# Kernel optimization log

Measured on AMD Instinct MI355X. Metric: run time of the kernel, lower is better.

Reference implementation:

```python
import jax, jax.numpy as jnp
import numpy as np

AR_COEF = 0.01
TAR_COEF = 0.01
LN_EPS = 1e-5


def setup_inputs() -> dict:
    key = jax.random.key(0)
    ks = jax.random.split(key, 8)
    B, T, D, E, H, A = 32, 512, 256, 1024, 1024, 64
    def rn(k, shape, fan_in):
        return jax.random.normal(k, shape, jnp.float32) * (1.0 / np.sqrt(fan_in))
    return {
        "obs": jax.random.normal(ks[0], (B, T, D), jnp.float32),
        "hxs": jnp.zeros((B, H), jnp.float32),
        "cxs": jnp.zeros((B, H), jnp.float32),
        "W1": rn(ks[1], (E, D), D), "b1": jnp.zeros((E,), jnp.float32),
        "W2": rn(ks[2], (E, E), E), "b2": jnp.zeros((E,), jnp.float32),
        "W_ih": rn(ks[3], (4 * H, E), E),
        "W_hh": rn(ks[4], (4 * H, H), H),
        "b_ih": jnp.zeros((4 * H,), jnp.float32),
        "b_hh": jnp.zeros((4 * H,), jnp.float32),
        "ln_g": jnp.ones((H,), jnp.float32), "ln_b": jnp.zeros((H,), jnp.float32),
        "Wa": rn(ks[5], (A, H), H), "ba": jnp.zeros((A,), jnp.float32),
        "Wc": rn(ks[6], (1, H), H), "bc": jnp.zeros((1,), jnp.float32),
    }


def reference(obs, hxs, cxs, W1, b1, W2, b2, W_ih, W_hh, b_ih, b_hh,
              ln_g, ln_b, Wa, ba, Wc, bc):
    # obs encoder (identity) + 2-layer SiLU MLP encoder
    enc = jax.nn.silu(obs @ W1.T + b1)        # (B,T,E)
    enc = jax.nn.silu(enc @ W2.T + b2)        # (B,T,E)

    # precompute input-to-gate contributions; gates in PyTorch order i,f,g,o
    x_gates = enc @ W_ih.T + (b_ih + b_hh)    # (B,T,4H)
    xg = jnp.transpose(x_gates, (1, 0, 2))    # (T,B,4H)

    def step(carry, xt):
        h, c = carry
        g = xt + h @ W_hh.T                   # (B,4H)
        i, f, gg, o = jnp.split(g, 4, axis=-1)
        c = jax.nn.sigmoid(f) * c + jax.nn.sigmoid(i) * jnp.tanh(gg)
        h = jax.nn.sigmoid(o) * jnp.tanh(c)
        return (h, c), h

    (h_n, c_n), outs = jax.lax.scan(step, (hxs, cxs), xg)
    out = jnp.transpose(outs, (1, 0, 2))      # (B,T,H)

    # LayerNorm
    mu = out.mean(-1, keepdims=True)
    var = ((out - mu) ** 2).mean(-1, keepdims=True)
    out_ln = (out - mu) * jax.lax.rsqrt(var + LN_EPS) * ln_g + ln_b

    ar_loss = (out_ln ** 2).mean() * AR_COEF
    tar_loss = ((out_ln[:, 1:, :] - out_ln[:, :-1, :]) ** 2).mean() * TAR_COEF

    logits = out_ln @ Wa.T + ba               # (B,T,A)
    values = (out_ln @ Wc.T + bc)[..., 0]     # (B,T)
    return logits, values, h_n, c_n, ar_loss, tar_loss
```

## Files before the change

kernel.cpp:

```cpp
#include <hip/hip_runtime.h>

typedef __attribute__((ext_vector_type(8))) short bf16x8;
typedef __attribute__((ext_vector_type(8))) unsigned short u16x8;
typedef __attribute__((ext_vector_type(4))) unsigned short u16x4;
typedef __attribute__((ext_vector_type(4))) float f32x4;

#define NB 32
#define NT 512
#define ND 256
#define NE 1024
#define NH 1024
#define LSTM_SMEM (131072 + 16640)

__device__ __forceinline__ float bf2f(unsigned short u){
  union { unsigned int i; float f; } w; w.i = ((unsigned int)u) << 16; return w.f;
}
__device__ __forceinline__ unsigned short f2bf(float f){
  union { float f; unsigned int i; } w; w.f = f;
  unsigned int r = (w.i >> 16) & 1u;
  return (unsigned short)((w.i + 0x7fffu + r) >> 16);
}

__device__ __forceinline__ f32x4 bypass_load_f32x4(const float* p){
  f32x4 r;
  asm volatile("global_load_dwordx4 %0, %1, off sc0 sc1" : "=v"(r) : "v"(p) : "memory");
  return r;
}
__device__ __forceinline__ int bypass_load_i32(const int* p){
  int r;
  asm volatile("global_load_dword %0, %1, off sc0 sc1\n\ts_waitcnt vmcnt(0)"
               : "=v"(r) : "v"(p) : "memory");
  return r;
}
__device__ __forceinline__ void bypass_store_f32x4(float* p, f32x4 v){
  asm volatile("global_store_dwordx4 %0, %1, off sc0 sc1" :: "v"(p), "v"(v) : "memory");
}

__device__ __forceinline__ void gload_lds16(const void* g, void* l){
  __builtin_amdgcn_global_load_lds(
      (const __attribute__((address_space(1))) void*)g,
      (__attribute__((address_space(3))) void*)l, 16, 0, 0);
}

__device__ __forceinline__ unsigned pkbf(float a, float b){
  unsigned r; asm("v_cvt_pk_bf16_f32 %0, %1, %2" : "=v"(r) : "v"(a), "v"(b)); return r;
}
__device__ __forceinline__ void make_frags(f32x4 x0, f32x4 x1, bf16x8& hi, bf16x8& lo){
  union Uv { unsigned u[4]; bf16x8 v; } H, L;
#pragma unroll
  for (int w=0; w<4; w++){
    float a = (w<2) ? x0[w*2]   : x1[(w-2)*2];
    float b = (w<2) ? x0[w*2+1] : x1[(w-2)*2+1];
    unsigned hw = pkbf(a, b);
    H.u[w] = hw;
    union { unsigned u; float f; } e0, e1;
    e0.u = hw << 16; e1.u = hw & 0xffff0000u;
    L.u[w] = pkbf(a - e0.f, b - e1.f);
  }
  hi = H.v; lo = L.v;
}

__global__ void mega_prep(const float* __restrict__ W1, const float* __restrict__ W2,
                          const float* __restrict__ Wih,
                          const float* __restrict__ Wa, const float* __restrict__ Wc,
                          const float* __restrict__ ba, const float* __restrict__ bc,
                          const float* __restrict__ b_ih, const float* __restrict__ b_hh,
                          const float* __restrict__ hxs, const float* __restrict__ cxs,
                          unsigned short* __restrict__ W1_b, unsigned short* __restrict__ W2_b,
                          unsigned short* __restrict__ Wih_b, unsigned short* __restrict__ Whead_b,
                          float* __restrict__ bias_heads, float* __restrict__ bias_xg,
                          float* __restrict__ h_bufs, float* __restrict__ c_buf,
                          int* __restrict__ cnt)
{
  long i0 = (long)blockIdx.x*256 + threadIdx.x;
  long stride = (long)gridDim.x*256;
  for (long i=i0; i<(long)NE*ND;   i+=stride) W1_b[i]  = f2bf(W1[i]);
  for (long i=i0; i<(long)NE*NE;   i+=stride) W2_b[i]  = f2bf(W2[i]);
  for (long i=i0; i<(long)4*NH*NE; i+=stride) Wih_b[i] = f2bf(Wih[i]);
  for (long i=i0; i<128*1024; i+=stride){
    int n = (int)(i>>10), k = (int)(i&1023);
    Whead_b[i] = f2bf(n<64 ? Wa[i] : (n==64 ? Wc[k] : 0.f));
  }
  for (long i=i0; i<4096; i+=stride) bias_xg[i] = b_ih[i] + b_hh[i];
  for (long i=i0; i<65;   i+=stride) bias_heads[i] = (i<64) ? ba[i] : bc[0];
  for (long i=i0; i<NB*NH; i+=stride){ h_bufs[i] = hxs[i]; c_buf[i] = cxs[i]; }
  for (long i=i0; i<1024; i+=stride) cnt[i] = 0;
}

__global__ void f2b_obs_chunk(const float* __restrict__ obs, unsigned short* __restrict__ dst,
                              int lgTc, int t0){
  const int Tc = 1 << lgTc;
  const long n = (long)NB * Tc * ND;
  long i = (long)blockIdx.x*blockDim.x + threadIdx.x;
  long stride = (long)gridDim.x*blockDim.x;
  for (; i < n; i += stride){
    long lr = i >> 8;
    int col = (int)(i & 255);
    long gr = (lr >> lgTc)*NT + t0 + (lr & (Tc-1));
    dst[i] = f2bf(obs[gr*ND + col]);
  }
}

__global__ void sentinel_kernel(float* __restrict__ out){ out[0] = 1.0e6f; }

#define GEMM_COMPUTE(P) { \
  bf16x8 af[4], bfr[4]; \
  _Pragma("unroll") for (int f=0; f<4; f++){ \
    af[f]  = *(const bf16x8*)&As[P][(wm*64 + f*16 + fr)*32 + kf]; \
    bfr[f] = *(const bf16x8*)&Bs[P][(wn*64 + f*16 + fr)*32 + kf]; } \
  _Pragma("unroll") for (int i=0;i<4;i++) \
    _Pragma("unroll") for (int j=0;j<4;j++) \
      acc[i][j] = __builtin_amdgcn_mfma_f32_16x16x32_bf16(af[i], bfr[j], acc[i][j], 0, 0, 0); }

template<int SILU, int HEADS>
__global__ __launch_bounds__(256)
void gemm_bt(const unsigned short* __restrict__ A, const unsigned short* __restrict__ Bw,
             const float* __restrict__ bias, unsigned short* __restrict__ C,
             float* __restrict__ oLogits, float* __restrict__ oValues,
             int K, int N, int Nreal)
{
  __shared__ __align__(16) unsigned short As[2][128*32];
  __shared__ __align__(16) unsigned short Bs[2][128*32];
  const int tid = threadIdx.x;
  const int lane = tid & 63;
  const int w = tid >> 6;
  const int wm = w >> 1, wn = w & 1;
  const int m0 = blockIdx.x * 128, n0 = blockIdx.y * 128;
  f32x4 acc[4][4];
#pragma unroll
  for (int i=0;i<4;i++)
#pragma unroll
    for (int j=0;j<4;j++){ f32x4 z = {0.f,0.f,0.f,0.f}; acc[i][j] = z; }
  const int fr = lane & 15;
  const int kf = (lane >> 4) * 8;
  const int r0 = tid >> 2, s0 = tid & 3;
  const unsigned short* gA0 = A  + (size_t)(m0+r0)*K    + s0*8;
  const unsigned short* gA1 = A  + (size_t)(m0+r0+64)*K + s0*8;
  const unsigned short* gB0 = Bw + (size_t)(n0+r0)*K    + s0*8;
  const unsigned short* gB1 = Bw + (size_t)(n0+r0+64)*K + s0*8;

  auto stage = [&](int p, int k0){
    char* a = (char*)&As[p][0] + w*1024;
    char* b = (char*)&Bs[p][0] + w*1024;
    gload_lds16(gA0 + k0, a);
    gload_lds16(gA1 + k0, a + 4096);
    gload_lds16(gB0 + k0, b);
    gload_lds16(gB1 + k0, b + 4096);
  };

  stage(0, 0);
  asm volatile("s_waitcnt vmcnt(0)" ::: "memory");
  __syncthreads();
  int cur = 0;
  for (int k0 = 32; k0 < K; k0 += 32){
    stage(cur ^ 1, k0);
    GEMM_COMPUTE(cur);
    asm volatile("s_waitcnt vmcnt(0)" ::: "memory");
    __syncthreads();
    cur ^= 1;
  }
  GEMM_COMPUTE(cur);

  const int mb = (lane >> 4) * 4;
  const int nb = lane & 15;
#pragma unroll
  for (int i=0;i<4;i++)
#pragma unroll
    for (int j=0;j<4;j++)
#pragma unroll
      for (int r=0;r<4;r++){
        int m = m0 + wm*64 + i*16 + mb + r;
        int n = n0 + wn*64 + j*16 + nb;
        if (HEADS && n >= Nreal) continue;
        float v = acc[i][j][r] + bias[n];
        if (SILU) v = v / (1.f + expf(-v));
        if (!HEADS) {
          C[(size_t)m*N + n] = f2bf(v);
        } else {
          if (n < 64) oLogits[(size_t)m*64 + n] = v;
          else if (n == 64) oValues[m] = v;
        }
      }
}

__global__ __launch_bounds__(512)
void lstm_mfma(const unsigned short* __restrict__ xg, const float* __restrict__ Whh,
               float* __restrict__ h_bufs, float* __restrict__ c_buf,
               unsigned short* __restrict__ hist, float* __restrict__ dh, float* __restrict__ dc,
               int* __restrict__ cnt, int t0, int t1, int Tc)
{
  extern __shared__ char smem[];
  unsigned short* Wf = (unsigned short*)smem;
  float* red = (float*)(smem + 131072);
  const int wg = blockIdx.x;
  const int bh = wg & 1, ug = wg >> 1;
  const int b0 = bh*16, n0w = ug*8;
  const int tid = threadIdx.x;
  const int lane = tid & 63;
  const int wv = tid >> 6;
  const int fr = lane & 15;
  const int q8 = (lane >> 4) * 8;

  for (int s = tid; s < 8192; s += 512){
    int term = s >> 12, kt = (s >> 7) & 31, nt = (s >> 6) & 1, l = s & 63;
    int r = nt*16 + (l & 15);
    int g = r >> 3, uu2 = r & 7;
    const float* src = Whh + (size_t)(g*NH + n0w + uu2)*NH + kt*32 + (l>>4)*8;
    u16x8 o;
#pragma unroll
    for (int j=0;j<8;j++){
      float wv_ = src[j];
      unsigned short hi = f2bf(wv_);
      o[j] = (term==0) ? hi : f2bf(wv_ - bf2f(hi));
    }
    *(u16x8*)&Wf[(size_t)s*8] = o;
  }

  const int bl = tid >> 3;
  const int uu = tid & 7;
  float c_reg = 0.f, h_keep = 0.f;
  if (tid < 128) c_reg = c_buf[(b0 + bl)*NH + n0w + uu];
  __syncthreads();

  for (int t = t0; t < t1; t++){
    const float* hb = h_bufs + (size_t)(t & 1)*(NB*NH);
    float* hb_next  = h_bufs + (size_t)((t+1)&1)*(NB*NH);
    const int tl = t - t0;

    float xgv[4] = {0.f,0.f,0.f,0.f};
    if (tid < 128){
      size_t xbase = ((size_t)(b0+bl)*Tc + tl)*4096 + n0w + uu;
#pragma unroll
      for (int g=0; g<4; g++) xgv[g] = bf2f(xg[xbase + g*1024]);
    }

    if (wv == 0){
      const int target = 256*t;
      while (true){
        int v = 0;
        if (lane < 16) v = bypass_load_i32(&cnt[lane*64]);
        v += __shfl_xor(v,1); v += __shfl_xor(v,2); v += __shfl_xor(v,4);
        v += __shfl_xor(v,8); v += __shfl_xor(v,16); v += __shfl_xor(v,32);
        if (v >= target) break;
        __builtin_amdgcn_s_sleep(1);
      }
    }
    __syncthreads();

    f32x4 hv[8];
#pragma unroll
    for (int ks=0; ks<4; ks++){
      const float* p = hb + (size_t)(b0 + fr)*NH + (wv*4 + ks)*32 + q8;
      hv[ks*2]   = bypass_load_f32x4(p);
      hv[ks*2+1] = bypass_load_f32x4(p + 4);
    }
    asm volatile("s_waitcnt vmcnt(0)" ::: "memory");
    __builtin_amdgcn_sched_barrier(0);

    bf16x8 ahi[4], alo[4];
#pragma unroll
    for (int ks=0; ks<4; ks++) make_frags(hv[2*ks], hv[2*ks+1], ahi[ks], alo[ks]);

    f32x4 acc[2];
    { f32x4 z = {0.f,0.f,0.f,0.f}; acc[0] = z; acc[1] = z; }
#pragma unroll
    for (int ks=0; ks<4; ks++){
      int kt = wv*4 + ks;
#pragma unroll
      for (int nt=0; nt<2; nt++){
        bf16x8 bhi = *(const bf16x8*)&Wf[kt*1024 + nt*512 + lane*8];
        bf16x8 blo = *(const bf16x8*)&Wf[32768 + kt*1024 + nt*512 + lane*8];
        acc[nt] = __builtin_amdgcn_mfma_f32_16x16x32_bf16(ahi[ks], bhi, acc[nt], 0,0,0);
        acc[nt] = __builtin_amdgcn_mfma_f32_16x16x32_bf16(ahi[ks], blo, acc[nt], 0,0,0);
        acc[nt] = __builtin_amdgcn_mfma_f32_16x16x32_bf16(alo[ks], bhi, acc[nt], 0,0,0);
      }
    }

#pragma unroll
    for (int nt=0; nt<2; nt++)
#pragma unroll
      for (int r4=0; r4<4; r4++)
        red[((lane>>4)*4 + r4)*260 + (nt*16 + fr)*8 + wv] = acc[nt][r4];
    __syncthreads();

    if (tid < 128){
      float gate[4];
#pragma unroll
      for (int g=0; g<4; g++){
        int base = bl*260 + (g*8 + uu)*8;
        f32x4 s0 = *(const f32x4*)&red[base];
        f32x4 s1 = *(const f32x4*)&red[base+4];
        gate[g] = ((s0[0]+s0[1])+(s0[2]+s0[3])) + ((s1[0]+s1[1])+(s1[2]+s1[3])) + xgv[g];
      }
      float iv = 1.f/(1.f+expf(-gate[0]));
      float fv = 1.f/(1.f+expf(-gate[1]));
      float gv = tanhf(gate[2]);
      float ov = 1.f/(1.f+expf(-gate[3]));
      float c_new = fv*c_reg + iv*gv;
      float h_new = ov*tanhf(c_new);
      c_reg = c_new; h_keep = h_new;
      float h0 = __shfl(h_new, (lane & 60) + 0);
      float h1 = __shfl(h_new, (lane & 60) + 1);
      float h2 = __shfl(h_new, (lane & 60) + 2);
      float h3 = __shfl(h_new, (lane & 60) + 3);
      if ((uu & 3) == 0){
        f32x4 hvv = { h0, h1, h2, h3 };
        bypass_store_f32x4(hb_next + (size_t)(b0+bl)*NH + n0w + uu, hvv);
        u16x4 hp; hp[0]=f2bf(h0); hp[1]=f2bf(h1); hp[2]=f2bf(h2); hp[3]=f2bf(h3);
        *(u16x4*)&hist[((size_t)(b0+bl)*Tc + tl)*NH + n0w + uu] = hp;
      }
    }
    __syncthreads();
    if (tid == 0) atomicAdd(&cnt[(wg & 15)*64], 1);
  }
  if (tid < 128){
    c_buf[(b0+bl)*NH + n0w + uu] = c_reg;
    if (t1 == NT){ dh[(b0+bl)*NH + n0w + uu] = h_keep; dc[(b0+bl)*NH + n0w + uu] = c_reg; }
  }
}

#define SEL4(A0,A1,A2,A3) ((kc&2)?((kc&1)?(A3):(A2)):((kc&1)?(A1):(A0)))

__global__ __launch_bounds__(512)
void lstm_valu(const unsigned short* __restrict__ xg, const float* __restrict__ Whh,
               float* __restrict__ h_bufs, float* __restrict__ c_buf,
               unsigned short* __restrict__ hist, float* __restrict__ dh, float* __restrict__ dc,
               int* __restrict__ cnt, int t0, int t1, int Tc)
{
  __shared__ __align__(16) float Wl[16*1024];
  const int wg = blockIdx.x;
  const int n0w = wg * 4;
  const int tid = threadIdx.x;
  const int lane = tid & 63;
  const int wv = tid >> 6;
  const int kc = lane & 15;
  const int b = wv*4 + (lane >> 4);

  for (int i = tid*4; i < 16*1024; i += 2048){
    int r = i >> 10, k = i & 1023;
    int grow = (r>>2)*NH + n0w + (r&3);
    *(f32x4*)&Wl[i] = *(const f32x4*)&Whh[(size_t)grow*NH + k];
  }
  float c_reg = 0.f, h_keep = 0.f;
  if (kc < 4) c_reg = c_buf[b*NH + n0w + kc];
  __syncthreads();

  for (int t = t0; t < t1; t++){
    const float* hb = h_bufs + (size_t)(t&1)*(NB*NH);
    float* hb_next  = h_bufs + (size_t)((t+1)&1)*(NB*NH);
    const int tl = t - t0;
    float xgi=0.f, xgf=0.f, xgg=0.f, xgo=0.f;
    if (kc < 4){
      size_t xbase = ((size_t)b*Tc + tl)*4096 + n0w + kc;
      xgi = bf2f(xg[xbase]);
      xgf = bf2f(xg[xbase + 1024]);
      xgg = bf2f(xg[xbase + 2048]);
      xgo = bf2f(xg[xbase + 3072]);
    }
    if (wv == 0){
      const int target = 256*t;
      while (true){
        int v = 0;
        if (lane < 16) v = bypass_load_i32(&cnt[lane*64]);
        v += __shfl_xor(v,1); v += __shfl_xor(v,2); v += __shfl_xor(v,4);
        v += __shfl_xor(v,8); v += __shfl_xor(v,16); v += __shfl_xor(v,32);
        if (v >= target) break;
        __builtin_amdgcn_s_sleep(1);
      }
    }
    __syncthreads();

    f32x4 hq[16];
    const float* hrow = hb + (size_t)b*NH + kc*4;
#pragma unroll
    for (int kk=0; kk<16; kk++) hq[kk] = bypass_load_f32x4(hrow + kk*64);

    float acc[16];
#pragma unroll
    for (int r=0;r<16;r++) acc[r] = 0.f;
#pragma unroll
    for (int g=0; g<4; g++){
      if (g==0){ asm volatile("s_waitcnt vmcnt(12)" ::: "memory"); }
      else if (g==1){ asm volatile("s_waitcnt vmcnt(8)" ::: "memory"); }
      else if (g==2){ asm volatile("s_waitcnt vmcnt(4)" ::: "memory"); }
      else { asm volatile("s_waitcnt vmcnt(0)" ::: "memory"); }
      __builtin_amdgcn_sched_barrier(0);
#pragma unroll
      for (int kq=0; kq<4; kq++){
        const int kk = g*4 + kq;
#pragma unroll
        for (int r=0;r<16;r++){
          f32x4 wq = *(const f32x4*)&Wl[r*1024 + kk*64 + kc*4];
          acc[r] = fmaf(wq[0],hq[kk][0], fmaf(wq[1],hq[kk][1],
                   fmaf(wq[2],hq[kk][2], fmaf(wq[3],hq[kk][3], acc[r]))));
        }
      }
    }
#pragma unroll
    for (int r=0;r<16;r++){
      float v = acc[r];
      v += __shfl_xor(v, 1);
      v += __shfl_xor(v, 2);
      v += __shfl_xor(v, 4);
      v += __shfl_xor(v, 8);
      acc[r] = v;
    }
    float gi = SEL4(acc[0], acc[1], acc[2], acc[3])   + xgi;
    float gf = SEL4(acc[4], acc[5], acc[6], acc[7])   + xgf;
    float gg = SEL4(acc[8], acc[9], acc[10], acc[11]) + xgg;
    float go = SEL4(acc[12],acc[13],acc[14],acc[15])  + xgo;
    float iv = 1.f/(1.f+expf(-gi));
    float fv = 1.f/(1.f+expf(-gf));
    float gv = tanhf(gg);
    float ov = 1.f/(1.f+expf(-go));
    float c_new = fv*c_reg + iv*gv;
    float h_new = ov*tanhf(c_new);
    if (kc < 4){ c_reg = c_new; h_keep = h_new; }
    const int base = lane & 48;
    float h0 = __shfl(h_new, base + 0);
    float h1 = __shfl(h_new, base + 1);
    float h2 = __shfl(h_new, base + 2);
    float h3 = __shfl(h_new, base + 3);
    if (kc == 0){
      f32x4 hvv = { h0, h1, h2, h3 };
      bypass_store_f32x4(hb_next + (size_t)b*NH + n0w, hvv);
      u16x4 hp;
      hp[0] = f2bf(h0); hp[1] = f2bf(h1); hp[2] = f2bf(h2); hp[3] = f2bf(h3);
      *(u16x4*)&hist[((size_t)b*Tc + tl)*NH + n0w] = hp;
    }
    asm volatile("s_waitcnt vmcnt(0)" ::: "memory");
    __syncthreads();
    if (tid == 0) atomicAdd(&cnt[(wg & 15) * 64], 1);
  }
  if (kc < 4){
    c_buf[b*NH + n0w + kc] = c_reg;
    if (t1 == NT){ dh[b*NH + n0w + kc] = h_keep; dc[b*NH + n0w + kc] = c_reg; }
  }
}

__global__ __launch_bounds__(256)
void ln_chunk(const unsigned short* __restrict__ X, const float* __restrict__ gam, const float* __restrict__ bet,
              unsigned short* __restrict__ Y, int lgTc, int t0)
{
  const int row = blockIdx.x;
  const int Tc = 1 << lgTc;
  const int bl = row >> lgTc, tl = row & (Tc-1);
  const long grow = (long)bl*NT + t0 + tl;
  const int tid = threadIdx.x;
  u16x4 xv = *(const u16x4*)&X[(size_t)row*NH + tid*4];
  float v0 = bf2f(xv[0]), v1 = bf2f(xv[1]), v2 = bf2f(xv[2]), v3 = bf2f(xv[3]);
  float s = v0+v1+v2+v3;
  s += __shfl_xor(s,1); s += __shfl_xor(s,2); s += __shfl_xor(s,4);
  s += __shfl_xor(s,8); s += __shfl_xor(s,16); s += __shfl_xor(s,32);
  __shared__ float red[8];
  if ((tid & 63) == 0) red[tid >> 6] = s;
  __syncthreads();
  float mean = (red[0]+red[1]+red[2]+red[3]) * (1.0f/NH);
  float d0 = v0-mean, d1 = v1-mean, d2 = v2-mean, d3 = v3-mean;
  float q = d0*d0 + d1*d1 + d2*d2 + d3*d3;
  q += __shfl_xor(q,1); q += __shfl_xor(q,2); q += __shfl_xor(q,4);
  q += __shfl_xor(q,8); q += __shfl_xor(q,16); q += __shfl_xor(q,32);
  if ((tid & 63) == 0) red[4 + (tid >> 6)] = q;
  __syncthreads();
  float var = (red[4]+red[5]+red[6]+red[7]) * (1.0f/NH);
  float rs = 1.f / sqrtf(var + 1e-5f);
  f32x4 gm = *(const f32x4*)&gam[tid*4];
  f32x4 bt = *(const f32x4*)&bet[tid*4];
  u16x4 ov;
  ov[0] = f2bf(d0*rs*gm[0] + bt[0]);
  ov[1] = f2bf(d1*rs*gm[1] + bt[1]);
  ov[2] = f2bf(d2*rs*gm[2] + bt[2]);
  ov[3] = f2bf(d3*rs*gm[3] + bt[3]);
  *(u16x4*)&Y[(size_t)grow*NH + tid*4] = ov;
}

__global__ __launch_bounds__(256)
void loss_partial(const unsigned short* __restrict__ Yu, float* __restrict__ partials)
{
  float ar = 0.f, tar = 0.f;
  long stride = (long)gridDim.x*256;
  for (long vv = (long)blockIdx.x*256 + threadIdx.x; vv < 2097152; vv += stride){
    long i = vv*8;
    int t = (int)((i >> 10) & 511);
    u16x8 y = *(const u16x8*)&Yu[i];
    float x[8];
#pragma unroll
    for (int q=0;q<8;q++){ x[q] = bf2f(y[q]); ar += x[q]*x[q]; }
    if (t > 0){
      u16x8 yp = *(const u16x8*)&Yu[i - 1024];
#pragma unroll
      for (int q=0;q<8;q++){ float d = x[q] - bf2f(yp[q]); tar += d*d; }
    }
  }
  ar += __shfl_xor(ar,1); ar += __shfl_xor(ar,2); ar += __shfl_xor(ar,4);
  ar += __shfl_xor(ar,8); ar += __shfl_xor(ar,16); ar += __shfl_xor(ar,32);
  tar += __shfl_xor(tar,1); tar += __shfl_xor(tar,2); tar += __shfl_xor(tar,4);
  tar += __shfl_xor(tar,8); tar += __shfl_xor(tar,16); tar += __shfl_xor(tar,32);
  __shared__ float red[16];
  int w = threadIdx.x >> 6;
  if ((threadIdx.x & 63) == 0){ red[w] = ar; red[8+w] = tar; }
  __syncthreads();
  if (threadIdx.x == 0){
    partials[blockIdx.x*2]   = red[0]+red[1]+red[2]+red[3];
    partials[blockIdx.x*2+1] = red[8]+red[9]+red[10]+red[11];
  }
}

__global__ __launch_bounds__(256)
void loss_final(const float* __restrict__ partials, float* __restrict__ oAr, float* __restrict__ oTar){
  double sa = 0.0, st = 0.0;
  for (int i = threadIdx.x; i < 1024; i += 256){ sa += (double)partials[2*i]; st += (double)partials[2*i+1]; }
  for (int m=1;m<64;m<<=1){ sa += __shfl_xor(sa, m); st += __shfl_xor(st, m); }
  __shared__ double rd[8];
  int w = threadIdx.x >> 6;
  if ((threadIdx.x & 63) == 0){ rd[w] = sa; rd[4+w] = st; }
  __syncthreads();
  if (threadIdx.x == 0){
    double a  = rd[0]+rd[1]+rd[2]+rd[3];
    double tt = rd[4]+rd[5]+rd[6]+rd[7];
    oAr[0]  = (float)(a  / 16777216.0 * 0.01);
    oTar[0] = (float)(tt / 16744448.0 * 0.01);
  }
}

extern "C" void kernel_launch(void* const* d_in, const int* in_sizes, int n_in,
                              void* d_out, int out_size, void* d_ws, size_t ws_size,
                              hipStream_t stream)
{
  const float* obs  = (const float*)d_in[0];
  const float* hxs  = (const float*)d_in[1];
  const float* cxs  = (const float*)d_in[2];
  const float* W1   = (const float*)d_in[3];
  const float* b1   = (const float*)d_in[4];
  const float* W2   = (const float*)d_in[5];
  const float* b2   = (const float*)d_in[6];
  const float* W_ih = (const float*)d_in[7];
  const float* W_hh = (const float*)d_in[8];
  const float* b_ih = (const float*)d_in[9];
  const float* b_hh = (const float*)d_in[10];
  const float* ln_g = (const float*)d_in[11];
  const float* ln_b = (const float*)d_in[12];
  const float* Wa   = (const float*)d_in[13];
  const float* ba   = (const float*)d_in[14];
  const float* Wc   = (const float*)d_in[15];
  const float* bc   = (const float*)d_in[16];

  char* ws = (char*)d_ws;
  size_t off = 0;
  auto alloc = [&](size_t bytes)->char*{
    char* p = ws + off;
    off = (off + bytes + 255) & ~(size_t)255;
    return p;
  };
  unsigned short* W1_b    = (unsigned short*)alloc((size_t)NE*ND*2);
  unsigned short* W2_b    = (unsigned short*)alloc((size_t)NE*NE*2);
  unsigned short* Wih_b   = (unsigned short*)alloc((size_t)4*NH*NE*2);
  unsigned short* Whead_b = (unsigned short*)alloc((size_t)128*NH*2);
  float* bias_heads       = (float*)alloc(65*4);
  float* bias_xg          = (float*)alloc(4096*4);
  unsigned short* outln_b = (unsigned short*)alloc((size_t)NB*NT*NH*2);
  float* h_bufs           = (float*)alloc((size_t)2*NB*NH*4);
  float* c_buf            = (float*)alloc((size_t)NB*NH*4);
  int*   cnt              = (int*)alloc(1024*4);
  float* partials         = (float*)alloc((size_t)1024*2*4);
  const size_t fixedEnd = off;

  int lg = -1;
  for (int L = 9; L >= 4; --L){
    size_t Mc = (size_t)NB << L;
    size_t per = Mc*ND*2 + 2*(Mc*NE*2) + Mc*4096*2 + Mc*NH*2 + 6*256;
    if (fixedEnd + per <= ws_size){ lg = L; break; }
  }
  if (lg < 0){ sentinel_kernel<<<1,1,0,stream>>>((float*)d_out); return; }
  const int Tc = 1 << lg;
  const int Mc = NB << lg;
  const int nChunks = NT >> lg;

  unsigned short* obs_c  = (unsigned short*)alloc((size_t)Mc*ND*2);
  unsigned short* enc1_c = (unsigned short*)alloc((size_t)Mc*NE*2);
  unsigned short* enc2_c = (unsigned short*)alloc((size_t)Mc*NE*2);
  unsigned short* xg_c   = (unsigned short*)alloc((size_t)Mc*4096*2);
  unsigned short* hist_c = (unsigned short*)alloc((size_t)Mc*NH*2);

  float* o = (float*)d_out;
  float* oLogits = o;
  float* oValues = o + (size_t)NB*NT*64;
  float* oH  = oValues + NB*NT;
  float* oC  = oH + NB*NH;
  float* oAr = oC + NB*NH;
  float* oTar= oAr + 1;

  mega_prep<<<2048,256,0,stream>>>(W1, W2, W_ih, Wa, Wc, ba, bc, b_ih, b_hh, hxs, cxs,
                                   W1_b, W2_b, Wih_b, Whead_b, bias_heads, bias_xg,
                                   h_bufs, c_buf, cnt);

  for (int c = 0; c < nChunks; ++c){
    int t0 = c << lg, t1 = t0 + Tc;
    f2b_obs_chunk<<<512,256,0,stream>>>(obs, obs_c, lg, t0);
    gemm_bt<1,0><<<dim3(Mc/128,8) ,256,0,stream>>>(obs_c,  W1_b,  b1,      enc1_c, nullptr, nullptr, ND, NE, NE);
    gemm_bt<1,0><<<dim3(Mc/128,8) ,256,0,stream>>>(enc1_c, W2_b,  b2,      enc2_c, nullptr, nullptr, NE, NE, NE);
    gemm_bt<0,0><<<dim3(Mc/128,32),256,0,stream>>>(enc2_c, Wih_b, bias_xg, xg_c,   nullptr, nullptr, NE, 4096, 4096);

    (void)hipGetLastError();
    lstm_mfma<<<256,512,LSTM_SMEM,stream>>>(xg_c, W_hh, h_bufs, c_buf, hist_c, oH, oC, cnt, t0, t1, Tc);
    if (hipGetLastError() != hipSuccess)
      lstm_valu<<<256,512,0,stream>>>(xg_c, W_hh, h_bufs, c_buf, hist_c, oH, oC, cnt, t0, t1, Tc);

    ln_chunk<<<Mc,256,0,stream>>>(hist_c, ln_g, ln_b, outln_b, lg, t0);
  }

  gemm_bt<0,1><<<dim3(128,1),256,0,stream>>>(outln_b, Whead_b, bias_heads, nullptr, oLogits, oValues, NH, 128, 65);
  loss_partial<<<1024,256,0,stream>>>(outln_b, partials);
  loss_final<<<1,256,0,stream>>>(partials, oAr, oTar);
}
```

Before: 2.617 ms.

## Replace global atomic counter barrier with per-block step flags and per-wave waits

The LSTM recurrence's inter-block barrier changes from atomic counters summed by one wave to per-workgroup flag words that store the completed step. Each wave polls only the 16 producer blocks whose h slices it reads, which drops a __syncthreads and the global all-to-all dependency. Gate work is spread across waves (16 lanes per wave) with a padded reduction buffer to reduce LDS bank conflicts. LayerNorm is rewritten to one row per wave with wider vector loads. The partial-dependency flags raise the risk of subtle memory-ordering bugs.

New measurement: 2.567 ms. About the same (-1.9%).

```diff
diff --git a/kernel.cpp b/kernel.cpp
--- a/kernel.cpp
+++ b/kernel.cpp
@@ -10,7 +10,7 @@
 #define ND 256
 #define NE 1024
 #define NH 1024
-#define LSTM_SMEM (131072 + 16640)
+#define LSTM_SMEM (131072 + 18432)
 
 __device__ __forceinline__ float bf2f(unsigned short u){
   union { unsigned int i; float f; } w; w.i = ((unsigned int)u) << 16; return w.f;
@@ -34,6 +34,9 @@
 }
 __device__ __forceinline__ void bypass_store_f32x4(float* p, f32x4 v){
   asm volatile("global_store_dwordx4 %0, %1, off sc0 sc1" :: "v"(p), "v"(v) : "memory");
+}
+__device__ __forceinline__ void bypass_store_i32(int* p, int v){
+  asm volatile("global_store_dword %0, %1, off sc0 sc1" :: "v"(p), "v"(v) : "memory");
 }
 
 __device__ __forceinline__ void gload_lds16(const void* g, void* l){
@@ -70,7 +73,7 @@
                           unsigned short* __restrict__ Wih_b, unsigned short* __restrict__ Whead_b,
                           float* __restrict__ bias_heads, float* __restrict__ bias_xg,
                           float* __restrict__ h_bufs, float* __restrict__ c_buf,
-                          int* __restrict__ cnt)
+                          int* __restrict__ flags)
 {
   long i0 = (long)blockIdx.x*256 + threadIdx.x;
   long stride = (long)gridDim.x*256;
@@ -84,7 +87,7 @@
   for (long i=i0; i<4096; i+=stride) bias_xg[i] = b_ih[i] + b_hh[i];
   for (long i=i0; i<65;   i+=stride) bias_heads[i] = (i<64) ? ba[i] : bc[0];
   for (long i=i0; i<NB*NH; i+=stride){ h_bufs[i] = hxs[i]; c_buf[i] = cxs[i]; }
-  for (long i=i0; i<1024; i+=stride) cnt[i] = 0;
+  for (long i=i0; i<8192; i+=stride) flags[i] = 0;
 }
 
 __global__ void f2b_obs_chunk(const float* __restrict__ obs, unsigned short* __restrict__ dst,
@@ -187,7 +190,7 @@
 void lstm_mfma(const unsigned short* __restrict__ xg, const float* __restrict__ Whh,
                float* __restrict__ h_bufs, float* __restrict__ c_buf,
                unsigned short* __restrict__ hist, float* __restrict__ dh, float* __restrict__ dc,
-               int* __restrict__ cnt, int t0, int t1, int Tc)
+               int* __restrict__ flags, int t0, int t1, int Tc)
 {
   extern __shared__ char smem[];
   unsigned short* Wf = (unsigned short*)smem;
@@ -216,10 +219,10 @@
     *(u16x8*)&Wf[(size_t)s*8] = o;
   }
 
-  const int bl = tid >> 3;
-  const int uu = tid & 7;
+  const int bl = wv*2 + (lane >> 3);
+  const int uu = lane & 7;
   float c_reg = 0.f, h_keep = 0.f;
-  if (tid < 128) c_reg = c_buf[(b0 + bl)*NH + n0w + uu];
+  if (lane < 16) c_reg = c_buf[(b0 + bl)*NH + n0w + uu];
   __syncthreads();
 
   for (int t = t0; t < t1; t++){
@@ -228,24 +231,24 @@
     const int tl = t - t0;
 
     float xgv[4] = {0.f,0.f,0.f,0.f};
-    if (tid < 128){
+    if (lane < 16){
       size_t xbase = ((size_t)(b0+bl)*Tc + tl)*4096 + n0w + uu;
 #pragma unroll
       for (int g=0; g<4; g++) xgv[g] = bf2f(xg[xbase + g*1024]);
     }
 
-    if (wv == 0){
-      const int target = 256*t;
+    {
+      const int pw = ((wv*16 + fr)*2 + bh) * 32;
       while (true){
-        int v = 0;
-        if (lane < 16) v = bypass_load_i32(&cnt[lane*64]);
-        v += __shfl_xor(v,1); v += __shfl_xor(v,2); v += __shfl_xor(v,4);
-        v += __shfl_xor(v,8); v += __shfl_xor(v,16); v += __shfl_xor(v,32);
-        if (v >= target) break;
+        int v = bypass_load_i32(&flags[pw]);
+        v = min(v, __shfl_xor(v, 1));
+        v = min(v, __shfl_xor(v, 2));
+        v = min(v, __shfl_xor(v, 4));
+        v = min(v, __shfl_xor(v, 8));
+        if (v >= t) break;
         __builtin_amdgcn_s_sleep(1);
       }
     }
-    __syncthreads();
 
     f32x4 hv[8];
 #pragma unroll
@@ -279,18 +282,21 @@
 #pragma unroll
     for (int nt=0; nt<2; nt++)
 #pragma unroll
-      for (int r4=0; r4<4; r4++)
-        red[((lane>>4)*4 + r4)*260 + (nt*16 + fr)*8 + wv] = acc[nt][r4];
+      for (int r4=0; r4<4; r4++){
+        int batch = (lane>>4)*4 + r4;
+        red[batch*288 + (nt*16 + fr)*9 + wv] = acc[nt][r4];
+      }
     __syncthreads();
 
-    if (tid < 128){
+    if (lane < 16){
       float gate[4];
 #pragma unroll
       for (int g=0; g<4; g++){
-        int base = bl*260 + (g*8 + uu)*8;
-        f32x4 s0 = *(const f32x4*)&red[base];
-        f32x4 s1 = *(const f32x4*)&red[base+4];
-        gate[g] = ((s0[0]+s0[1])+(s0[2]+s0[3])) + ((s1[0]+s1[1])+(s1[2]+s1[3])) + xgv[g];
+        const float* rp = &red[bl*288 + (g*8 + uu)*9];
+        float s = 0.f;
+#pragma unroll
+        for (int w8=0; w8<8; w8++) s += rp[w8];
+        gate[g] = s + xgv[g];
       }
       float iv = 1.f/(1.f+expf(-gate[0]));
       float fv = 1.f/(1.f+expf(-gate[1]));
@@ -299,11 +305,11 @@
       float c_new = fv*c_reg + iv*gv;
       float h_new = ov*tanhf(c_new);
       c_reg = c_new; h_keep = h_new;
-      float h0 = __shfl(h_new, (lane & 60) + 0);
-      float h1 = __shfl(h_new, (lane & 60) + 1);
-      float h2 = __shfl(h_new, (lane & 60) + 2);
-      float h3 = __shfl(h_new, (lane & 60) + 3);
-      if ((uu & 3) == 0){
+      float h0 = __shfl(h_new, (lane & ~3) + 0);
+      float h1 = __shfl(h_new, (lane & ~3) + 1);
+      float h2 = __shfl(h_new, (lane & ~3) + 2);
+      float h3 = __shfl(h_new, (lane & ~3) + 3);
+      if ((lane & 3) == 0){
         f32x4 hvv = { h0, h1, h2, h3 };
         bypass_store_f32x4(hb_next + (size_t)(b0+bl)*NH + n0w + uu, hvv);
         u16x4 hp; hp[0]=f2bf(h0); hp[1]=f2bf(h1); hp[2]=f2bf(h2); hp[3]=f2bf(h3);
@@ -311,9 +317,9 @@
       }
     }
     __syncthreads();
-    if (tid == 0) atomicAdd(&cnt[(wg & 15)*64], 1);
-  }
-  if (tid < 128){
+    if (tid == 0) bypass_store_i32(&flags[wg*32], t+1);
+  }
+  if (lane < 16){
     c_buf[(b0+bl)*NH + n0w + uu] = c_reg;
     if (t1 == NT){ dh[(b0+bl)*NH + n0w + uu] = h_keep; dc[(b0+bl)*NH + n0w + uu] = c_reg; }
   }
@@ -442,36 +448,46 @@
 void ln_chunk(const unsigned short* __restrict__ X, const float* __restrict__ gam, const float* __restrict__ bet,
               unsigned short* __restrict__ Y, int lgTc, int t0)
 {
-  const int row = blockIdx.x;
   const int Tc = 1 << lgTc;
+  const int row = blockIdx.x*4 + (threadIdx.x >> 6);
+  const int lane = threadIdx.x & 63;
   const int bl = row >> lgTc, tl = row & (Tc-1);
   const long grow = (long)bl*NT + t0 + tl;
-  const int tid = threadIdx.x;
-  u16x4 xv = *(const u16x4*)&X[(size_t)row*NH + tid*4];
-  float v0 = bf2f(xv[0]), v1 = bf2f(xv[1]), v2 = bf2f(xv[2]), v3 = bf2f(xv[3]);
-  float s = v0+v1+v2+v3;
+  u16x8 a0 = *(const u16x8*)&X[(size_t)row*NH + lane*16];
+  u16x8 a1 = *(const u16x8*)&X[(size_t)row*NH + lane*16 + 8];
+  float x[16];
+  float s = 0.f;
+#pragma unroll
+  for (int j=0;j<8;j++){ x[j] = bf2f(a0[j]); x[8+j] = bf2f(a1[j]); }
+#pragma unroll
+  for (int j=0;j<16;j++) s += x[j];
   s += __shfl_xor(s,1); s += __shfl_xor(s,2); s += __shfl_xor(s,4);
   s += __shfl_xor(s,8); s += __shfl_xor(s,16); s += __shfl_xor(s,32);
-  __shared__ float red[8];
-  if ((tid & 63) == 0) red[tid >> 6] = s;
-  __syncthreads();
-  float mean = (red[0]+red[1]+red[2]+red[3]) * (1.0f/NH);
-  float d0 = v0-mean, d1 = v1-mean, d2 = v2-mean, d3 = v3-mean;
-  float q = d0*d0 + d1*d1 + d2*d2 + d3*d3;
+  const float mean = s * (1.0f/NH);
+  float q = 0.f;
+#pragma unroll
+  for (int j=0;j<16;j++){ float d = x[j]-mean; q += d*d; }
   q += __shfl_xor(q,1); q += __shfl_xor(q,2); q += __shfl_xor(q,4);
   q += __shfl_xor(q,8); q += __shfl_xor(q,16); q += __shfl_xor(q,32);
-  if ((tid & 63) == 0) red[4 + (tid >> 6)] = q;
-  __syncthreads();
-  float var = (red[4]+red[5]+red[6]+red[7]) * (1.0f/NH);
-  float rs = 1.f / sqrtf(var + 1e-5f);
-  f32x4 gm = *(const f32x4*)&gam[tid*4];
-  f32x4 bt = *(const f32x4*)&bet[tid*4];
-  u16x4 ov;
-  ov[0] = f2bf(d0*rs*gm[0] + bt[0]);
-  ov[1] = f2bf(d1*rs*gm[1] + bt[1]);
-  ov[2] = f2bf(d2*rs*gm[2] + bt[2]);
-  ov[3] = f2bf(d3*rs*gm[3] + bt[3]);
-  *(u16x4*)&Y[(size_t)grow*NH + tid*4] = ov;
+  const float rs = 1.f / sqrtf(q * (1.0f/NH) + 1e-5f);
+  f32x4 g0 = *(const f32x4*)&gam[lane*16];
+  f32x4 g1 = *(const f32x4*)&gam[lane*16+4];
+  f32x4 g2 = *(const f32x4*)&gam[lane*16+8];
+  f32x4 g3 = *(const f32x4*)&gam[lane*16+12];
+  f32x4 b0 = *(const f32x4*)&bet[lane*16];
+  f32x4 b1 = *(const f32x4*)&bet[lane*16+4];
+  f32x4 b2 = *(const f32x4*)&bet[lane*16+8];
+  f32x4 b3 = *(const f32x4*)&bet[lane*16+12];
+  u16x8 o0, o1;
+#pragma unroll
+  for (int j=0;j<4;j++){
+    o0[j]   = f2bf((x[j]   -mean)*rs*g0[j] + b0[j]);
+    o0[4+j] = f2bf((x[4+j] -mean)*rs*g1[j] + b1[j]);
+    o1[j]   = f2bf((x[8+j] -mean)*rs*g2[j] + b2[j]);
+    o1[4+j] = f2bf((x[12+j]-mean)*rs*g3[j] + b3[j]);
+  }
+  *(u16x8*)&Y[(size_t)grow*NH + lane*16]     = o0;
+  *(u16x8*)&Y[(size_t)grow*NH + lane*16 + 8] = o1;
 }
 
 __global__ __launch_bounds__(256)
@@ -561,7 +577,7 @@
   unsigned short* outln_b = (unsigned short*)alloc((size_t)NB*NT*NH*2);
   float* h_bufs           = (float*)alloc((size_t)2*NB*NH*4);
   float* c_buf            = (float*)alloc((size_t)NB*NH*4);
-  int*   cnt              = (int*)alloc(1024*4);
+  int*   flags            = (int*)alloc(8192*4);
   float* partials         = (float*)alloc((size_t)1024*2*4);
   const size_t fixedEnd = off;
 
@@ -592,7 +608,7 @@
 
   mega_prep<<<2048,256,0,stream>>>(W1, W2, W_ih, Wa, Wc, ba, bc, b_ih, b_hh, hxs, cxs,
                                    W1_b, W2_b, Wih_b, Whead_b, bias_heads, bias_xg,
-                                   h_bufs, c_buf, cnt);
+                                   h_bufs, c_buf, flags);
 
   for (int c = 0; c < nChunks; ++c){
     int t0 = c << lg, t1 = t0 + Tc;
@@ -602,11 +618,11 @@
     gemm_bt<0,0><<<dim3(Mc/128,32),256,0,stream>>>(enc2_c, Wih_b, bias_xg, xg_c,   nullptr, nullptr, NE, 4096, 4096);
 
     (void)hipGetLastError();
-    lstm_mfma<<<256,512,LSTM_SMEM,stream>>>(xg_c, W_hh, h_bufs, c_buf, hist_c, oH, oC, cnt, t0, t1, Tc);
+    lstm_mfma<<<256,512,LSTM_SMEM,stream>>>(xg_c, W_hh, h_bufs, c_buf, hist_c, oH, oC, flags, t0, t1, Tc);
     if (hipGetLastError() != hipSuccess)
-      lstm_valu<<<256,512,0,stream>>>(xg_c, W_hh, h_bufs, c_buf, hist_c, oH, oC, cnt, t0, t1, Tc);
-
-    ln_chunk<<<Mc,256,0,stream>>>(hist_c, ln_g, ln_b, outln_b, lg, t0);
+      lstm_valu<<<256,512,0,stream>>>(xg_c, W_hh, h_bufs, c_buf, hist_c, oH, oC, flags, t0, t1, Tc);
+
+    ln_chunk<<<Mc/4,256,0,stream>>>(hist_c, ln_g, ln_b, outln_b, lg, t0);
   }
 
   gemm_bt<0,1><<<dim3(128,1),256,0,stream>>>(outln_b, Whead_b, bias_heads, nullptr, oLogits, oValues, NH, 128, 65);
```
